# Kernel optimization log

Measured on AMD Instinct MI355X. Metric: run time of the kernel, lower is better.

Reference implementation:

```python
import jax, jax.numpy as jnp
import numpy as np

B, S, H, L = 64, 512, 768, 9


def setup_inputs() -> dict:
    key = jax.random.key(0)
    ks = jax.random.split(key, 8)
    hidden = jax.random.normal(ks[0], (B, S, H), jnp.float32)
    lengths = jax.random.randint(ks[1], (B,), S // 2, S + 1)
    attention_mask = (jnp.arange(S)[None, :] < lengths[:, None]).astype(jnp.int32)
    labels = jax.random.randint(ks[2], (B, S), 0, L)
    # sprinkle some -100 ignore labels like HF datasets do
    ignore = jax.random.uniform(ks[3], (B, S)) < 0.05
    labels = jnp.where(ignore, -100, labels)
    W = jax.random.normal(ks[4], (H, L), jnp.float32) * 0.02
    b = jnp.zeros((L,), jnp.float32)
    start_transitions = jax.random.uniform(ks[5], (L,), jnp.float32, -0.1, 0.1)
    end_transitions = jax.random.uniform(ks[6], (L,), jnp.float32, -0.1, 0.1)
    transitions = jax.random.uniform(ks[7], (L, L), jnp.float32, -0.1, 0.1)
    return dict(hidden=hidden, attention_mask=attention_mask, labels=labels, W=W, b=b,
                start_transitions=start_transitions, end_transitions=end_transitions,
                transitions=transitions)


def _crf_numerator(emissions, tags, maskf, start_t, end_t, trans):
    # score of the gold tag sequence (torchcrf _compute_score)
    first = start_t[tags[:, 0]] + jnp.take_along_axis(emissions[:, 0], tags[:, 0:1], axis=1)[:, 0]
    em = jnp.take_along_axis(emissions, tags[..., None], axis=2)[..., 0]      # [B,S]
    tr = trans[tags[:, :-1], tags[:, 1:]]                                     # [B,S-1]
    score = first + jnp.sum((em[:, 1:] + tr) * maskf[:, 1:], axis=1)
    last_idx = (jnp.sum(maskf, axis=1).astype(jnp.int32) - 1)
    last_tags = jnp.take_along_axis(tags, last_idx[:, None], axis=1)[:, 0]
    return score + end_t[last_tags]


def _crf_lognorm(emissions, maskf, start_t, end_t, trans):
    # forward algorithm (torchcrf _compute_normalizer) as a lax.scan
    score0 = start_t[None, :] + emissions[:, 0]                               # [B,L]
    em_seq = jnp.transpose(emissions[:, 1:], (1, 0, 2))                       # [S-1,B,L]
    m_seq = maskf[:, 1:].T                                                    # [S-1,B]

    def step(score, xs):
        em_t, m_t = xs
        nxt = jax.nn.logsumexp(score[:, :, None] + trans[None] + em_t[:, None, :], axis=1)
        return jnp.where(m_t[:, None] > 0, nxt, score), None

    score, _ = jax.lax.scan(step, score0, (em_seq, m_seq))
    return jax.nn.logsumexp(score + end_t[None, :], axis=1)


def _viterbi(emissions, maskf, start_t, end_t, trans):
    score0 = start_t[None, :] + emissions[:, 0]                               # [B,L]
    em_seq = jnp.transpose(emissions[:, 1:], (1, 0, 2))
    m_seq = maskf[:, 1:].T

    def step(score, xs):
        em_t, m_t = xs
        cand = score[:, :, None] + trans[None]                                # [B,L,L]
        bp = jnp.argmax(cand, axis=1)                                         # [B,L]
        nxt = jnp.max(cand, axis=1) + em_t
        return jnp.where(m_t[:, None] > 0, nxt, score), bp

    score, history = jax.lax.scan(step, score0, (em_seq, m_seq))              # history [S-1,B,L]
    best_last = jnp.argmax(score + end_t[None, :], axis=1)                    # [B]

    def back(cur, xs):
        bp_t, m_t = xs
        prev = jnp.where(m_t > 0, jnp.take_along_axis(bp_t, cur[:, None], axis=1)[:, 0], cur)
        return prev, prev

    _, tags_rev = jax.lax.scan(back, best_last, (history[::-1], m_seq[::-1]))
    tags = jnp.concatenate([tags_rev[::-1].T, best_last[:, None]], axis=1)    # [B,S]
    return tags


def reference(hidden, attention_mask, labels, W, b, start_transitions, end_transitions, transitions):
    maskf = attention_mask.astype(hidden.dtype)                               # [B,S]
    logits = jnp.einsum('bsh,hl->bsl', hidden, W) + b                         # [B,S,L]
    safe_labels = jnp.where(labels == -100, 0, labels)
    num = _crf_numerator(logits, safe_labels, maskf, start_transitions, end_transitions, transitions)
    den = _crf_lognorm(logits, maskf, start_transitions, end_transitions, transitions)
    loss = -jnp.mean(num - den)                                               # -crf(..., reduction='mean')
    tags = _viterbi(logits, maskf, start_transitions, end_transitions, transitions)
    fake_logits = jax.nn.one_hot(tags, L, dtype=logits.dtype) * maskf[..., None]
    return loss, fake_logits
```

## Files before the change

### kernel.cpp

```cpp
#include <hip/hip_runtime.h>
#include <hip/hip_bf16.h>

constexpr int BB  = 64;
constexpr int SS  = 512;
constexpr int HH  = 768;
constexpr int NL  = 9;
constexpr int NROWS = BB * SS;
constexpr int EMN   = SS * NL;

__global__ __launch_bounds__(256, 2) void logits_kernel(
    const float* __restrict__ hidden, const float* __restrict__ W,
    const float* __restrict__ bias, float* __restrict__ logits) {
  const int lane   = threadIdx.x & 63;
  const int wid    = blockIdx.x * (blockDim.x >> 6) + (threadIdx.x >> 6);
  const int nwaves = gridDim.x * (blockDim.x >> 6);

  float w[3][4][NL];
#pragma unroll
  for (int j = 0; j < 3; ++j)
#pragma unroll
    for (int k = 0; k < 4; ++k) {
      const int r = lane * 4 + j * 256 + k;
#pragma unroll
      for (int l = 0; l < NL; ++l) w[j][k][l] = W[r * NL + l];
    }
  const float my_bias = (lane < NL) ? bias[lane] : 0.0f;

  for (int row = wid; row < NROWS; row += nwaves) {
    const float4* hp = (const float4*)(hidden + (size_t)row * HH);
    float acc[NL];
#pragma unroll
    for (int l = 0; l < NL; ++l) acc[l] = 0.0f;
#pragma unroll
    for (int j = 0; j < 3; ++j) {
      const float4 h = hp[lane + j * 64];
#pragma unroll
      for (int l = 0; l < NL; ++l)
        acc[l] += h.x * w[j][0][l] + h.y * w[j][1][l] +
                  h.z * w[j][2][l] + h.w * w[j][3][l];
    }
#pragma unroll
    for (int off = 32; off >= 1; off >>= 1)
#pragma unroll
      for (int l = 0; l < NL; ++l) acc[l] += __shfl_xor(acc[l], off, 64);
    if (lane < NL) {
      float v = acc[0];
#pragma unroll
      for (int l = 1; l < NL; ++l) if (lane == l) v = acc[l];
      logits[(size_t)row * NL + lane] = v + my_bias;
    }
  }
}

__global__ __launch_bounds__(64) void crf_kernel(
    const float* __restrict__ logits, const int* __restrict__ mask,
    const int* __restrict__ labels, const float* __restrict__ start_t,
    const float* __restrict__ end_t, const float* __restrict__ trans,
    float* __restrict__ out, float* __restrict__ num_den) {
  __shared__ float em[EMN];
  __shared__ float tr_s[NL * NL];
  __shared__ int   lab[SS];
  __shared__ unsigned char bp[EMN];
  __shared__ unsigned char tags[SS];
  __shared__ int   len_s;

  const int role = blockIdx.x >> 6;
  const int b    = blockIdx.x & 63;
  const int tid  = threadIdx.x;

  for (int i = tid; i < EMN; i += 64) em[i] = logits[(size_t)b * EMN + i];
  for (int i = tid; i < NL * NL; i += 64) tr_s[i] = trans[i];
  int lsum = 0;
  for (int t = tid; t < SS; t += 64) lsum += mask[b * SS + t];
#pragma unroll
  for (int off = 32; off >= 1; off >>= 1) lsum += __shfl_xor(lsum, off, 64);
  if (tid == 0) len_s = lsum;
  if (role == 2) {
    for (int t = tid; t < SS; t += 64) {
      const int v = labels[b * SS + t];
      lab[t] = (v == -100) ? 0 : v;
    }
  }
  __syncthreads();
  const int len = len_s;

  if (role == 0) {
    const int j = (tid < NL) ? tid : 0;
    float tcol[NL];
#pragma unroll
    for (int i = 0; i < NL; ++i) tcol[i] = tr_s[i * NL + j];
    float s[NL];
#pragma unroll
    for (int i = 0; i < NL; ++i) s[i] = start_t[i] + em[i];
    for (int t = 1; t < len; ++t) {
      float c[NL];
#pragma unroll
      for (int i = 0; i < NL; ++i) c[i] = s[i] + tcol[i];
      float m = c[0];
#pragma unroll
      for (int i = 1; i < NL; ++i) m = fmaxf(m, c[i]);
      float sum = 0.0f;
#pragma unroll
      for (int i = 0; i < NL; ++i) sum += __expf(c[i] - m);
      const float nxt = m + __logf(sum) + em[t * NL + j];
#pragma unroll
      for (int i = 0; i < NL; ++i) s[i] = __shfl(nxt, i, 64);
    }
    float c[NL];
#pragma unroll
    for (int i = 0; i < NL; ++i) c[i] = s[i] + end_t[i];
    float m = c[0];
#pragma unroll
    for (int i = 1; i < NL; ++i) m = fmaxf(m, c[i]);
    float sum = 0.0f;
#pragma unroll
    for (int i = 0; i < NL; ++i) sum += __expf(c[i] - m);
    if (tid == 0) num_den[64 + b] = m + __logf(sum);

  } else if (role == 1) {
    const int j = (tid < NL) ? tid : 0;
    float tcol[NL];
#pragma unroll
    for (int i = 0; i < NL; ++i) tcol[i] = tr_s[i * NL + j];
    float s[NL];
#pragma unroll
    for (int i = 0; i < NL; ++i) s[i] = start_t[i] + em[i];
    for (int t = 1; t < len; ++t) {
      float best = s[0] + tcol[0];
      int   arg  = 0;
#pragma unroll
      for (int i = 1; i < NL; ++i) {
        const float c = s[i] + tcol[i];
        if (c > best) { best = c; arg = i; }
      }
      if (tid < NL) bp[t * NL + j] = (unsigned char)arg;
      const float nxt = best + em[t * NL + j];
#pragma unroll
      for (int i = 0; i < NL; ++i) s[i] = __shfl(nxt, i, 64);
    }
    int   bl = 0;
    float bv = s[0] + end_t[0];
#pragma unroll
    for (int i = 1; i < NL; ++i) {
      const float c = s[i] + end_t[i];
      if (c > bv) { bv = c; bl = i; }
    }
    __syncthreads();
    if (tid == 0) {
      int cur = bl;
      for (int t = SS - 1; t >= len - 1; --t) tags[t] = (unsigned char)cur;
      for (int t = len - 1; t >= 1; --t) {
        cur = bp[t * NL + cur];
        tags[t - 1] = (unsigned char)cur;
      }
    }
    __syncthreads();
    for (int idx = tid; idx < EMN; idx += 64) {
      const int t = idx / NL;
      const int l = idx - t * NL;
      out[1 + (size_t)b * EMN + idx] =
          (t < len && l == (int)tags[t]) ? 1.0f : 0.0f;
    }

  } else {
    float contrib = 0.0f;
    for (int t = tid; t < SS; t += 64) {
      if (t >= 1 && t < len)
        contrib += em[t * NL + lab[t]] + tr_s[lab[t - 1] * NL + lab[t]];
    }
#pragma unroll
    for (int off = 32; off >= 1; off >>= 1)
      contrib += __shfl_xor(contrib, off, 64);
    if (tid == 0) {
      const int l0 = lab[0];
      num_den[b] = start_t[l0] + em[l0] + contrib + end_t[lab[len - 1]];
    }
  }
}

__global__ __launch_bounds__(64) void loss_kernel(
    const float* __restrict__ num_den, float* __restrict__ out) {
  const int tid = threadIdx.x;
  float v = num_den[64 + tid] - num_den[tid];
#pragma unroll
  for (int off = 32; off >= 1; off >>= 1) v += __shfl_xor(v, off, 64);
  if (tid == 0) out[0] = v * (1.0f / 64.0f);
}

extern "C" void kernel_launch(void* const* d_in, const int* in_sizes, int n_in,
                              void* d_out, int out_size, void* d_ws, size_t ws_size,
                              hipStream_t stream) {
  const float* hidden  = (const float*)d_in[0];
  const int*   mask    = (const int*)d_in[1];
  const int*   labels  = (const int*)d_in[2];
  const float* W       = (const float*)d_in[3];
  const float* bias    = (const float*)d_in[4];
  const float* start_t = (const float*)d_in[5];
  const float* end_t   = (const float*)d_in[6];
  const float* trans   = (const float*)d_in[7];
  float* out = (float*)d_out;

  float* logits  = (float*)d_ws;
  float* num_den = logits + (size_t)NROWS * NL;

  logits_kernel<<<1024, 256, 0, stream>>>(hidden, W, bias, logits);
  crf_kernel<<<192, 64, 0, stream>>>(logits, mask, labels, start_t, end_t,
                                     trans, out, num_den);
  loss_kernel<<<1, 64, 0, stream>>>(num_den, out);
}
```

Before: 281.7 us.

## Rework logits GEMV tiling and CRF recurrences with exp2, readlane, parallel backtrace

Result: slower. 292.0 us (+3.7%).

```diff
diff --git a/kernel.cpp b/kernel.cpp
--- a/kernel.cpp
+++ b/kernel.cpp
@@ -1,5 +1,6 @@
 #include <hip/hip_runtime.h>
 #include <hip/hip_bf16.h>
+#include <stdint.h>
 
 constexpr int BB  = 64;
 constexpr int SS  = 512;
@@ -7,13 +8,21 @@
 constexpr int NL  = 9;
 constexpr int NROWS = BB * SS;
 constexpr int EMN   = SS * NL;
+constexpr float L2E = 1.4426950408889634f;
+constexpr float LN2 = 0.6931471805599453f;
+
+__device__ __forceinline__ float readlane_f(float v, int lane) {
+  union { float f; int i; } u;
+  u.f = v;
+  u.i = __builtin_amdgcn_readlane(u.i, lane);
+  return u.f;
+}
 
 __global__ __launch_bounds__(256, 2) void logits_kernel(
     const float* __restrict__ hidden, const float* __restrict__ W,
     const float* __restrict__ bias, float* __restrict__ logits) {
-  const int lane   = threadIdx.x & 63;
-  const int wid    = blockIdx.x * (blockDim.x >> 6) + (threadIdx.x >> 6);
-  const int nwaves = gridDim.x * (blockDim.x >> 6);
+  const int lane = threadIdx.x & 63;
+  const int wid  = blockIdx.x * 4 + (threadIdx.x >> 6);
 
   float w[3][4][NL];
 #pragma unroll
@@ -26,28 +35,41 @@
     }
   const float my_bias = (lane < NL) ? bias[lane] : 0.0f;
 
-  for (int row = wid; row < NROWS; row += nwaves) {
-    const float4* hp = (const float4*)(hidden + (size_t)row * HH);
-    float acc[NL];
-#pragma unroll
-    for (int l = 0; l < NL; ++l) acc[l] = 0.0f;
+#pragma unroll
+  for (int rep = 0; rep < 2; ++rep) {
+    const int rA = wid + rep * 16384;
+    const int rB = rA + 8192;
+    const float4* hA = (const float4*)(hidden + (size_t)rA * HH);
+    const float4* hB = (const float4*)(hidden + (size_t)rB * HH);
+    float accA[NL], accB[NL];
+#pragma unroll
+    for (int l = 0; l < NL; ++l) { accA[l] = 0.0f; accB[l] = 0.0f; }
 #pragma unroll
     for (int j = 0; j < 3; ++j) {
-      const float4 h = hp[lane + j * 64];
-#pragma unroll
-      for (int l = 0; l < NL; ++l)
-        acc[l] += h.x * w[j][0][l] + h.y * w[j][1][l] +
-                  h.z * w[j][2][l] + h.w * w[j][3][l];
+      const float4 a = hA[lane + j * 64];
+      const float4 b = hB[lane + j * 64];
+#pragma unroll
+      for (int l = 0; l < NL; ++l) {
+        accA[l] += a.x * w[j][0][l] + a.y * w[j][1][l] +
+                   a.z * w[j][2][l] + a.w * w[j][3][l];
+        accB[l] += b.x * w[j][0][l] + b.y * w[j][1][l] +
+                   b.z * w[j][2][l] + b.w * w[j][3][l];
+      }
     }
 #pragma unroll
     for (int off = 32; off >= 1; off >>= 1)
 #pragma unroll
-      for (int l = 0; l < NL; ++l) acc[l] += __shfl_xor(acc[l], off, 64);
+      for (int l = 0; l < NL; ++l) {
+        accA[l] += __shfl_xor(accA[l], off, 64);
+        accB[l] += __shfl_xor(accB[l], off, 64);
+      }
     if (lane < NL) {
-      float v = acc[0];
-#pragma unroll
-      for (int l = 1; l < NL; ++l) if (lane == l) v = acc[l];
-      logits[(size_t)row * NL + lane] = v + my_bias;
+      float vA = accA[0], vB = accB[0];
+#pragma unroll
+      for (int l = 1; l < NL; ++l)
+        if (lane == l) { vA = accA[l]; vB = accB[l]; }
+      logits[(size_t)rA * NL + lane] = vA + my_bias;
+      logits[(size_t)rB * NL + lane] = vB + my_bias;
     }
   }
 }
@@ -57,19 +79,28 @@
     const int* __restrict__ labels, const float* __restrict__ start_t,
     const float* __restrict__ end_t, const float* __restrict__ trans,
     float* __restrict__ out, float* __restrict__ num_den) {
-  __shared__ float em[EMN];
+  __shared__ __align__(16) float em_s[EMN + 16];
   __shared__ float tr_s[NL * NL];
   __shared__ int   lab[SS];
-  __shared__ unsigned char bp[EMN];
-  __shared__ unsigned char tags[SS];
+  __shared__ unsigned char bp_s[EMN + 80];
+  __shared__ unsigned char tags_s[SS];
   __shared__ int   len_s;
 
   const int role = blockIdx.x >> 6;
   const int b    = blockIdx.x & 63;
   const int tid  = threadIdx.x;
-
-  for (int i = tid; i < EMN; i += 64) em[i] = logits[(size_t)b * EMN + i];
-  for (int i = tid; i < NL * NL; i += 64) tr_s[i] = trans[i];
+  const float esc = (role == 0) ? L2E : 1.0f;
+
+  {
+    const float4* src = (const float4*)(logits + (size_t)b * EMN);
+    float4* dst = (float4*)em_s;
+    for (int i = tid; i < EMN / 4; i += 64) {
+      float4 v = src[i];
+      v.x *= esc; v.y *= esc; v.z *= esc; v.w *= esc;
+      dst[i] = v;
+    }
+  }
+  for (int i = tid; i < NL * NL; i += 64) tr_s[i] = trans[i] * esc;
   int lsum = 0;
   for (int t = tid; t < SS; t += 64) lsum += mask[b * SS + t];
 #pragma unroll
@@ -91,31 +122,37 @@
     for (int i = 0; i < NL; ++i) tcol[i] = tr_s[i * NL + j];
     float s[NL];
 #pragma unroll
-    for (int i = 0; i < NL; ++i) s[i] = start_t[i] + em[i];
+    for (int i = 0; i < NL; ++i) s[i] = start_t[i] * L2E + em_s[i];
+    float emj = em_s[NL + j];
     for (int t = 1; t < len; ++t) {
+      const float emj_n = em_s[(t + 1) * NL + j];
       float c[NL];
 #pragma unroll
       for (int i = 0; i < NL; ++i) c[i] = s[i] + tcol[i];
-      float m = c[0];
-#pragma unroll
-      for (int i = 1; i < NL; ++i) m = fmaxf(m, c[i]);
-      float sum = 0.0f;
-#pragma unroll
-      for (int i = 0; i < NL; ++i) sum += __expf(c[i] - m);
-      const float nxt = m + __logf(sum) + em[t * NL + j];
-#pragma unroll
-      for (int i = 0; i < NL; ++i) s[i] = __shfl(nxt, i, 64);
+      const float m01 = fmaxf(c[0], c[1]), m23 = fmaxf(c[2], c[3]);
+      const float m45 = fmaxf(c[4], c[5]), m67 = fmaxf(c[6], c[7]);
+      const float m = fmaxf(fmaxf(fmaxf(m01, m23), fmaxf(m45, m67)), c[8]);
+      float p[NL];
+#pragma unroll
+      for (int i = 0; i < NL; ++i) p[i] = exp2f(c[i] - m);
+      const float s01 = p[0] + p[1], s23 = p[2] + p[3];
+      const float s45 = p[4] + p[5], s67 = p[6] + p[7];
+      const float sum = ((s01 + s23) + (s45 + s67)) + p[8];
+      const float nxt = m + __log2f(sum) + emj;
+#pragma unroll
+      for (int i = 0; i < NL; ++i) s[i] = readlane_f(nxt, i);
+      emj = emj_n;
     }
     float c[NL];
 #pragma unroll
-    for (int i = 0; i < NL; ++i) c[i] = s[i] + end_t[i];
-    float m = c[0];
-#pragma unroll
-    for (int i = 1; i < NL; ++i) m = fmaxf(m, c[i]);
+    for (int i = 0; i < NL; ++i) c[i] = s[i] + end_t[i] * L2E;
+    const float m01 = fmaxf(c[0], c[1]), m23 = fmaxf(c[2], c[3]);
+    const float m45 = fmaxf(c[4], c[5]), m67 = fmaxf(c[6], c[7]);
+    const float m = fmaxf(fmaxf(fmaxf(m01, m23), fmaxf(m45, m67)), c[8]);
     float sum = 0.0f;
 #pragma unroll
-    for (int i = 0; i < NL; ++i) sum += __expf(c[i] - m);
-    if (tid == 0) num_den[64 + b] = m + __logf(sum);
+    for (int i = 0; i < NL; ++i) sum += exp2f(c[i] - m);
+    if (tid == 0) num_den[64 + b] = (m + __log2f(sum)) * LN2;
 
   } else if (role == 1) {
     const int j = (tid < NL) ? tid : 0;
@@ -124,56 +161,94 @@
     for (int i = 0; i < NL; ++i) tcol[i] = tr_s[i * NL + j];
     float s[NL];
 #pragma unroll
-    for (int i = 0; i < NL; ++i) s[i] = start_t[i] + em[i];
+    for (int i = 0; i < NL; ++i) s[i] = start_t[i] + em_s[i];
+    float emj = em_s[NL + j];
     for (int t = 1; t < len; ++t) {
-      float best = s[0] + tcol[0];
-      int   arg  = 0;
-#pragma unroll
-      for (int i = 1; i < NL; ++i) {
-        const float c = s[i] + tcol[i];
-        if (c > best) { best = c; arg = i; }
+      const float emj_n = em_s[(t + 1) * NL + j];
+      float c[NL];
+#pragma unroll
+      for (int i = 0; i < NL; ++i) c[i] = s[i] + tcol[i];
+      const bool b01 = c[0] >= c[1], b23 = c[2] >= c[3];
+      const bool b45 = c[4] >= c[5], b67 = c[6] >= c[7];
+      const float v01 = b01 ? c[0] : c[1]; const int i01 = b01 ? 0 : 1;
+      const float v23 = b23 ? c[2] : c[3]; const int i23 = b23 ? 2 : 3;
+      const float v45 = b45 ? c[4] : c[5]; const int i45 = b45 ? 4 : 5;
+      const float v67 = b67 ? c[6] : c[7]; const int i67 = b67 ? 6 : 7;
+      const bool bA = v01 >= v23, bB = v45 >= v67;
+      const float vA = bA ? v01 : v23; const int iA = bA ? i01 : i23;
+      const float vB = bB ? v45 : v67; const int iB = bB ? i45 : i67;
+      const bool bC = vA >= vB;
+      const float vC = bC ? vA : vB; const int iC = bC ? iA : iB;
+      const bool bD = vC >= c[8];
+      const float best = bD ? vC : c[8];
+      const int   arg  = bD ? iC : 8;
+      bp_s[t * NL + tid] = (unsigned char)arg;
+      const float nxt = best + emj;
+#pragma unroll
+      for (int i = 0; i < NL; ++i) s[i] = readlane_f(nxt, i);
+      emj = emj_n;
+    }
+    float bv = s[0] + end_t[0];
+    int   bl = 0;
+#pragma unroll
+    for (int i = 1; i < NL; ++i) {
+      const float cc = s[i] + end_t[i];
+      if (cc > bv) { bv = cc; bl = i; }
+    }
+    __syncthreads();
+
+    uint64_t C = 0x876543210ULL;
+#pragma unroll
+    for (int k = 1; k <= 8; ++k) {
+      const int t = 8 * tid + k;
+      uint64_t nc = 0;
+#pragma unroll
+      for (int x = 0; x < 9; ++x) {
+        const int g = bp_s[t * NL + x] & 15;
+        nc |= ((C >> (4 * g)) & 15ULL) << (4 * x);
       }
-      if (tid < NL) bp[t * NL + j] = (unsigned char)arg;
-      const float nxt = best + em[t * NL + j];
-#pragma unroll
-      for (int i = 0; i < NL; ++i) s[i] = __shfl(nxt, i, 64);
-    }
-    int   bl = 0;
-    float bv = s[0] + end_t[0];
-#pragma unroll
-    for (int i = 1; i < NL; ++i) {
-      const float c = s[i] + end_t[i];
-      if (c > bv) { bv = c; bl = i; }
+      C = (t < len) ? nc : C;
+    }
+    const uint32_t Clo = (uint32_t)C, Chi = (uint32_t)(C >> 32);
+    uint32_t cur = (uint32_t)bl;
+    int bnd = 0;
+#pragma unroll
+    for (int c = 63; c >= 0; --c) {
+      bnd = (tid == c) ? (int)cur : bnd;
+      const uint32_t lo = (uint32_t)__builtin_amdgcn_readlane((int)Clo, c);
+      const uint32_t hi = (uint32_t)__builtin_amdgcn_readlane((int)Chi, c);
+      const uint64_t cc = ((uint64_t)hi << 32) | lo;
+      cur = (uint32_t)((cc >> (4 * cur)) & 15u);
+    }
+    int tag = bnd;
+#pragma unroll
+    for (int k = 8; k >= 1; --k) {
+      const int t = 8 * tid + k;
+      const int tt = (t < 512) ? t : 511;
+      const int nt = bp_s[tt * NL + tag];
+      tag = (t < len) ? nt : tag;
+      tags_s[t - 1] = (unsigned char)tag;
     }
     __syncthreads();
-    if (tid == 0) {
-      int cur = bl;
-      for (int t = SS - 1; t >= len - 1; --t) tags[t] = (unsigned char)cur;
-      for (int t = len - 1; t >= 1; --t) {
-        cur = bp[t * NL + cur];
-        tags[t - 1] = (unsigned char)cur;
-      }
-    }
-    __syncthreads();
-    for (int idx = tid; idx < EMN; idx += 64) {
-      const int t = idx / NL;
-      const int l = idx - t * NL;
-      out[1 + (size_t)b * EMN + idx] =
-          (t < len && l == (int)tags[t]) ? 1.0f : 0.0f;
+    for (int i = tid; i < EMN; i += 64) {
+      const int t = i / NL;
+      const int l = i - t * NL;
+      out[1 + (size_t)b * EMN + i] =
+          (t < len && l == (int)tags_s[t]) ? 1.0f : 0.0f;
     }
 
   } else {
     float contrib = 0.0f;
     for (int t = tid; t < SS; t += 64) {
       if (t >= 1 && t < len)
-        contrib += em[t * NL + lab[t]] + tr_s[lab[t - 1] * NL + lab[t]];
+        contrib += em_s[t * NL + lab[t]] + tr_s[lab[t - 1] * NL + lab[t]];
     }
 #pragma unroll
     for (int off = 32; off >= 1; off >>= 1)
       contrib += __shfl_xor(contrib, off, 64);
     if (tid == 0) {
       const int l0 = lab[0];
-      num_den[b] = start_t[l0] + em[l0] + contrib + end_t[lab[len - 1]];
+      num_den[b] = start_t[l0] + em_s[l0] + contrib + end_t[lab[len - 1]];
     }
   }
 }
@@ -203,7 +278,7 @@
   float* logits  = (float*)d_ws;
   float* num_den = logits + (size_t)NROWS * NL;
 
-  logits_kernel<<<1024, 256, 0, stream>>>(hidden, W, bias, logits);
+  logits_kernel<<<2048, 256, 0, stream>>>(hidden, W, bias, logits);
   crf_kernel<<<192, 64, 0, stream>>>(logits, mask, labels, start_t, end_t,
                                      trans, out, num_den);
   loss_kernel<<<1, 64, 0, stream>>>(num_den, out);
```
